# Kernel tuning notes

Measured on AMD Instinct MI355X. Metric: run time of the kernel, lower is better.

Reference implementation:

```python
import jax, jax.numpy as jnp
import numpy as np

DIM = 1024
HEADS = 16
HEAD_DIM = DIM // HEADS


def setup_inputs() -> dict:
    key = jax.random.key(0)
    ks = jax.random.split(key, 5)
    s = 1.0 / np.sqrt(DIM)
    x = jax.random.normal(ks[0], (2, 2048, DIM), dtype=jnp.float32)
    # torch nn.Linear weights are [out_features, in_features]
    W_qkv = jax.random.uniform(ks[1], (3 * DIM, DIM), dtype=jnp.float32, minval=-s, maxval=s)
    b_qkv = jax.random.uniform(ks[2], (3 * DIM,), dtype=jnp.float32, minval=-s, maxval=s)
    W_out = jax.random.uniform(ks[3], (DIM, DIM), dtype=jnp.float32, minval=-s, maxval=s)
    b_out = jax.random.uniform(ks[4], (DIM,), dtype=jnp.float32, minval=-s, maxval=s)
    return {"x": x, "W_qkv": W_qkv, "b_qkv": b_qkv, "W_out": W_out, "b_out": b_out}


def reference(x, W_qkv, b_qkv, W_out, b_out):
    B, N, D = x.shape
    qkv = jnp.einsum('bnd,ed->bne', x, W_qkv) + b_qkv            # [B,N,3D]
    qkv = qkv.reshape(B, N, 3, HEADS, HEAD_DIM)
    qkv = jnp.transpose(qkv, (2, 0, 3, 1, 4))                    # [3,B,H,N,hd]
    q, k, v = qkv[0], qkv[1], qkv[2]
    scale = 1.0 / np.sqrt(HEAD_DIM).astype(np.float32)
    attn = jnp.einsum('bhnd,bhmd->bhnm', q, k) * scale           # [B,H,N,N]
    attn = jax.nn.softmax(attn, axis=-1)
    out = jnp.einsum('bhnm,bhmd->bhnd', attn, v)                 # [B,H,N,hd]
    out = jnp.transpose(out, (0, 2, 1, 3)).reshape(B, N, D)
    out = jnp.einsum('bnd,ed->bne', out, W_out) + b_out
    return out
```

## Files before the change

kernel.cpp:

```cpp
#include <hip/hip_runtime.h>
#include <stdint.h>
#include <stddef.h>

typedef __attribute__((ext_vector_type(4))) float  f32x4;
typedef __attribute__((ext_vector_type(8))) short  s16x8;
typedef __attribute__((ext_vector_type(4))) float  float4v;
typedef __attribute__((ext_vector_type(4))) unsigned short u16x4;
typedef __attribute__((ext_vector_type(2))) unsigned int   u32x2;

#define DIM    1024
#define HEADS  16
#define HD     64
#define SEQ    2048
#define BATCH  2
#define TOKENS (BATCH * SEQ)

#define QSCALE 0.18033688011112042f

__device__ __forceinline__ unsigned short f2bf(float f) {
  union { float f; uint32_t u; } x; x.f = f;
  uint32_t r = x.u + 0x7fffu + ((x.u >> 16) & 1u);
  return (unsigned short)(r >> 16);
}

__device__ __forceinline__ float fast_exp2(float x) {
#if __has_builtin(__builtin_amdgcn_exp2f)
  return __builtin_amdgcn_exp2f(x);
#else
  return exp2f(x);
#endif
}

__device__ __forceinline__ uint32_t pack_bf16_trunc(uint32_t lo, uint32_t hi) {
#if __has_builtin(__builtin_amdgcn_perm)
  return __builtin_amdgcn_perm(hi, lo, 0x07060302u);
#else
  return (hi & 0xffff0000u) | (lo >> 16);
#endif
}

__device__ __forceinline__ void stage16(const unsigned short* gp, unsigned short* lp) {
#if __has_builtin(__builtin_amdgcn_global_load_lds)
  __builtin_amdgcn_global_load_lds((const __attribute__((address_space(1))) void*)gp,
                                   (__attribute__((address_space(3))) void*)lp, 16, 0, 0);
#else
  *(s16x8*)(lp + (threadIdx.x & 63) * 8) = *(const s16x8*)gp;
#endif
}

#define N4_X  (TOKENS * DIM / 4)
#define N4_WQ (3 * DIM * DIM / 4)
#define N4_WO (DIM * DIM / 4)
__global__ __launch_bounds__(256) void mhsa_cast_all(const float* __restrict__ x,
    const float* __restrict__ wq, const float* __restrict__ wo,
    unsigned short* __restrict__ xb, unsigned short* __restrict__ wqb,
    unsigned short* __restrict__ wob) {
  int i = blockIdx.x * 256 + threadIdx.x;
  const float* src; unsigned short* dst; int off;
  if (i < N4_X)              { src = x;  dst = xb;  off = i; }
  else if (i < N4_X + N4_WQ) { src = wq; dst = wqb; off = i - N4_X; }
  else                       { src = wo; dst = wob; off = i - (N4_X + N4_WQ); }
  float4v f = ((const float4v*)src)[off];
  u16x4 o;
  o.x = f2bf(f.x); o.y = f2bf(f.y); o.z = f2bf(f.z); o.w = f2bf(f.w);
  ((u16x4*)dst)[off] = o;
}


__global__ __launch_bounds__(256, 3) void mhsa_gemm_qkv(const unsigned short* __restrict__ A,
    const unsigned short* __restrict__ Bw, const float* __restrict__ bias,
    unsigned short* __restrict__ qws, unsigned short* __restrict__ kws,
    unsigned short* __restrict__ vws) {
  __shared__ unsigned short As[2][128 * 32];
  __shared__ unsigned short Bs[2][128 * 32];
  const int t = threadIdx.x;
  const int w = t >> 6, l = t & 63;
  const int wm = w >> 1, wn = w & 1;
  const int rowBase = blockIdx.y * 128;
  const int colBase = blockIdx.x * 128;
  const int fr = l & 15, q4 = l >> 4, ln = l & 15;
  const int srow = l >> 2;
  const int scol = ((l & 3) ^ (srow & 3)) * 8;

  f32x4 zero = {0.f, 0.f, 0.f, 0.f};
  f32x4 acc[4][4];
  #pragma unroll
  for (int a = 0; a < 4; ++a)
    #pragma unroll
    for (int b = 0; b < 4; ++b) acc[a][b] = zero;

  #pragma unroll
  for (int it = 0; it < 2; ++it) {
    const int c = w * 2 + it;
    stage16(A  + (size_t)(rowBase + c * 16 + srow) * DIM + scol, &As[0][c * 512]);
    stage16(Bw + (size_t)(colBase + c * 16 + srow) * DIM + scol, &Bs[0][c * 512]);
  }
  __syncthreads();

  for (int kt = 0; kt < DIM / 32; ++kt) {
    const int cur = kt & 1, nxt = cur ^ 1;
    if (kt + 1 < DIM / 32) {
      const int k1 = (kt + 1) * 32;
      #pragma unroll
      for (int it = 0; it < 2; ++it) {
        const int c = w * 2 + it;
        stage16(A  + (size_t)(rowBase + c * 16 + srow) * DIM + k1 + scol, &As[nxt][c * 512]);
        stage16(Bw + (size_t)(colBase + c * 16 + srow) * DIM + k1 + scol, &Bs[nxt][c * 512]);
      }
    }
    s16x8 xf[4], wf[4];
    #pragma unroll
    for (int b = 0; b < 4; ++b)
      xf[b] = *(const s16x8*)&As[cur][(wm * 64 + b * 16 + fr) * 32 + ((q4 ^ (fr & 3)) * 8)];
    #pragma unroll
    for (int a = 0; a < 4; ++a)
      wf[a] = *(const s16x8*)&Bs[cur][(wn * 64 + a * 16 + fr) * 32 + ((q4 ^ (fr & 3)) * 8)];
    #pragma unroll
    for (int a = 0; a < 4; ++a)
      #pragma unroll
      for (int b = 0; b < 4; ++b)
        acc[a][b] = __builtin_amdgcn_mfma_f32_16x16x32_bf16(wf[a], xf[b], acc[a][b], 0, 0, 0);
    __syncthreads();
  }

  const int which = colBase >> 10;
  const float sc = (which == 0) ? QSCALE : 1.0f;
  unsigned short* dst = (which == 0) ? qws : ((which == 1) ? kws : vws);

  #pragma unroll
  for (int a = 0; a < 4; ++a) {
    const int e0 = colBase + wn * 64 + a * 16 + q4 * 4;
    const float4v bs4 = *(const float4v*)&bias[e0];
    const int rr0 = e0 & 1023;
    const int h = rr0 >> 6, d0 = rr0 & 63;
    #pragma unroll
    for (int b = 0; b < 4; ++b) {
      const int tok = rowBase + wm * 64 + b * 16 + ln;
      const int bb = tok >> 11, n = tok & 2047;
      if (which != 2) {
        u16x4 pk;
        #pragma unroll
        for (int r = 0; r < 4; ++r) pk[r] = f2bf((acc[a][b][r] + bs4[r]) * sc);
        *(u16x4*)&dst[(((size_t)(bb * HEADS + h)) * SEQ + n) * HD + d0] = pk;
      } else {
        #pragma unroll
        for (int r = 0; r < 4; ++r)
          dst[(((size_t)(bb * HEADS + h)) * HD + d0 + r) * SEQ + n] =
              f2bf(acc[a][b][r] + bs4[r]);
      }
    }
  }
}

__global__ __launch_bounds__(256, 3) void mhsa_gemm_out(const unsigned short* __restrict__ A,
    const unsigned short* __restrict__ Bw, const float* __restrict__ bias,
    float* __restrict__ out) {
  __shared__ unsigned short As[2][64 * 32];
  __shared__ unsigned short Bs[2][128 * 32];
  const int t = threadIdx.x;
  const int w = t >> 6, l = t & 63;
  const int wm = w >> 1, wn = w & 1;
  const int rowBase = blockIdx.y * 64;
  const int colBase = blockIdx.x * 128;
  const int fr = l & 15, q4 = l >> 4, ln = l & 15;
  const int srow = l >> 2;
  const int scol = ((l & 3) ^ (srow & 3)) * 8;

  f32x4 zero = {0.f, 0.f, 0.f, 0.f};
  f32x4 acc[4][2];
  #pragma unroll
  for (int a = 0; a < 4; ++a)
    #pragma unroll
    for (int b = 0; b < 2; ++b) acc[a][b] = zero;

  #pragma unroll
  for (int it = 0; it < 3; ++it) {
    const int s = w * 3 + it;
    if (s < 4) stage16(A  + (size_t)(rowBase + s * 16 + srow) * DIM + scol, &As[0][s * 512]);
    else       stage16(Bw + (size_t)(colBase + (s - 4) * 16 + srow) * DIM + scol, &Bs[0][(s - 4) * 512]);
  }
  __syncthreads();

  for (int kt = 0; kt < DIM / 32; ++kt) {
    const int cur = kt & 1, nxt = cur ^ 1;
    if (kt + 1 < DIM / 32) {
      const int k1 = (kt + 1) * 32;
      #pragma unroll
      for (int it = 0; it < 3; ++it) {
        const int s = w * 3 + it;
        if (s < 4) stage16(A  + (size_t)(rowBase + s * 16 + srow) * DIM + k1 + scol, &As[nxt][s * 512]);
        else       stage16(Bw + (size_t)(colBase + (s - 4) * 16 + srow) * DIM + k1 + scol, &Bs[nxt][(s - 4) * 512]);
      }
    }
    s16x8 xf[2], wf[4];
    #pragma unroll
    for (int b = 0; b < 2; ++b)
      xf[b] = *(const s16x8*)&As[cur][(wm * 32 + b * 16 + fr) * 32 + ((q4 ^ (fr & 3)) * 8)];
    #pragma unroll
    for (int a = 0; a < 4; ++a)
      wf[a] = *(const s16x8*)&Bs[cur][(wn * 64 + a * 16 + fr) * 32 + ((q4 ^ (fr & 3)) * 8)];
    #pragma unroll
    for (int a = 0; a < 4; ++a)
      #pragma unroll
      for (int b = 0; b < 2; ++b)
        acc[a][b] = __builtin_amdgcn_mfma_f32_16x16x32_bf16(wf[a], xf[b], acc[a][b], 0, 0, 0);
    __syncthreads();
  }

  #pragma unroll
  for (int a = 0; a < 4; ++a) {
    const int e0 = colBase + wn * 64 + a * 16 + q4 * 4;
    const float4v bs4 = *(const float4v*)&bias[e0];
    #pragma unroll
    for (int b = 0; b < 2; ++b) {
      const int tok = rowBase + wm * 32 + b * 16 + ln;
      float4v v;
      #pragma unroll
      for (int r = 0; r < 4; ++r) v[r] = acc[a][b][r] + bs4[r];
      *(float4v*)&out[(size_t)tok * DIM + e0] = v;
    }
  }
}

__global__ __launch_bounds__(256, 2) void mhsa_attn(const unsigned short* __restrict__ q,
    const unsigned short* __restrict__ k, const unsigned short* __restrict__ vt,
    unsigned short* __restrict__ o) {
  __shared__ unsigned short QPs[4 * 32 * 72];
  __shared__ unsigned short Ks[2][64 * 64];
  __shared__ unsigned short Vs[2][64 * 64];
  const int t = threadIdx.x, w = t >> 6, l = t & 63;
  const int q4 = l >> 4, ln = l & 15;
  const int bh = blockIdx.y, q0 = blockIdx.x * 128;
  const unsigned short* qb  = q  + (size_t)bh * SEQ * HD;
  const unsigned short* kb  = k  + (size_t)bh * SEQ * HD;
  const unsigned short* vtb = vt + (size_t)bh * HD * SEQ;

  const int srow = l >> 3;
  const int scol = ((l & 7) ^ srow) * 8;

  unsigned short* Pw = &QPs[w * (32 * 72)];

  #pragma unroll
  for (int it = 0; it < 4; ++it)
    stage16(qb + (size_t)(q0 + w * 32 + it * 8 + srow) * HD + scol, &Pw[it * 512]);
  #pragma unroll
  for (int it = 0; it < 2; ++it) {
    const int c = w + it * 4;
    stage16(kb  + (size_t)(c * 8 + srow) * HD + scol, &Ks[0][c * 512]);
    stage16(vtb + (size_t)(c * 8 + srow) * SEQ + scol, &Vs[0][c * 512]);
  }
  __syncthreads();

  s16x8 aq[2][2];
  #pragma unroll
  for (int i = 0; i < 2; ++i)
    #pragma unroll
    for (int kk = 0; kk < 2; ++kk)
      aq[i][kk] = *(const s16x8*)&Pw[(i * 16 + ln) * 64 + (((kk * 4 + q4) ^ (ln & 7)) * 8)];

  f32x4 zero = {0.f, 0.f, 0.f, 0.f};
  f32x4 accO[2][4];
  float lsum[2] = {0.f, 0.f};
  #pragma unroll
  for (int i = 0; i < 2; ++i)
    #pragma unroll
    for (int jd = 0; jd < 4; ++jd) accO[i][jd] = zero;

  for (int jt = 0; jt < SEQ / 64; ++jt) {
    const int cur = jt & 1, nxt = cur ^ 1;
    if (jt + 1 < SEQ / 64) {
      const int j1 = (jt + 1) * 64;
      #pragma unroll
      for (int it = 0; it < 2; ++it) {
        const int c = w + it * 4;
        stage16(kb  + (size_t)(j1 + c * 8 + srow) * HD + scol, &Ks[nxt][c * 512]);
        stage16(vtb + (size_t)(c * 8 + srow) * SEQ + j1 + scol, &Vs[nxt][c * 512]);
      }
    }

    f32x4 St[4][2];
    #pragma unroll
    for (int jb = 0; jb < 4; ++jb)
      #pragma unroll
      for (int i = 0; i < 2; ++i) St[jb][i] = zero;
    #pragma unroll
    for (int jb = 0; jb < 4; ++jb) {
      s16x8 ak0 = *(const s16x8*)&Ks[cur][(jb * 16 + ln) * 64 + ((q4 ^ (ln & 7)) * 8)];
      s16x8 ak1 = *(const s16x8*)&Ks[cur][(jb * 16 + ln) * 64 + (((4 + q4) ^ (ln & 7)) * 8)];
      #pragma unroll
      for (int i = 0; i < 2; ++i) {
        St[jb][i] = __builtin_amdgcn_mfma_f32_16x16x32_bf16(ak0, aq[i][0], St[jb][i], 0, 0, 0);
        St[jb][i] = __builtin_amdgcn_mfma_f32_16x16x32_bf16(ak1, aq[i][1], St[jb][i], 0, 0, 0);
      }
    }

    #pragma unroll
    for (int i = 0; i < 2; ++i)
      #pragma unroll
      for (int jb = 0; jb < 4; ++jb) {
        uint32_t u0 = __float_as_uint(fast_exp2(St[jb][i][0]));
        uint32_t u1 = __float_as_uint(fast_exp2(St[jb][i][1]));
        uint32_t u2 = __float_as_uint(fast_exp2(St[jb][i][2]));
        uint32_t u3 = __float_as_uint(fast_exp2(St[jb][i][3]));
        lsum[i] += __uint_as_float(u0 & 0xffff0000u) + __uint_as_float(u1 & 0xffff0000u)
                 + __uint_as_float(u2 & 0xffff0000u) + __uint_as_float(u3 & 0xffff0000u);
        u32x2 pk;
        pk.x = pack_bf16_trunc(u0, u1);
        pk.y = pack_bf16_trunc(u2, u3);
        *(u32x2*)&Pw[(i * 16 + ln) * 72 + jb * 16 + q4 * 4] = pk;
      }

    s16x8 ap[2][2];
    #pragma unroll
    for (int i = 0; i < 2; ++i)
      #pragma unroll
      for (int kk = 0; kk < 2; ++kk)
        ap[i][kk] = *(const s16x8*)&Pw[(i * 16 + ln) * 72 + kk * 32 + q4 * 8];

    #pragma unroll
    for (int jd = 0; jd < 4; ++jd) {
      s16x8 bv0 = *(const s16x8*)&Vs[cur][(jd * 16 + ln) * 64 + ((q4 ^ (ln & 7)) * 8)];
      s16x8 bv1 = *(const s16x8*)&Vs[cur][(jd * 16 + ln) * 64 + (((4 + q4) ^ (ln & 7)) * 8)];
      #pragma unroll
      for (int i = 0; i < 2; ++i) {
        accO[i][jd] = __builtin_amdgcn_mfma_f32_16x16x32_bf16(ap[i][0], bv0, accO[i][jd], 0, 0, 0);
        accO[i][jd] = __builtin_amdgcn_mfma_f32_16x16x32_bf16(ap[i][1], bv1, accO[i][jd], 0, 0, 0);
      }
    }

    __syncthreads();
  }

  const int b = bh >> 4, h = bh & 15;
  #pragma unroll
  for (int i = 0; i < 2; ++i) {
    float s = lsum[i];
    s += __shfl_xor(s, 16);
    s += __shfl_xor(s, 32);
    const float inv = 1.f / s;
    #pragma unroll
    for (int r = 0; r < 4; ++r) {
      const float invr = __shfl(inv, (l & 48) + q4 * 4 + r);
      const int row = q0 + w * 32 + i * 16 + q4 * 4 + r;
      #pragma unroll
      for (int jd = 0; jd < 4; ++jd)
        o[((size_t)(b * SEQ + row)) * DIM + h * HD + jd * 16 + ln] = f2bf(accO[i][jd][r] * invr);
    }
  }
}

extern "C" void kernel_launch(void* const* d_in, const int* in_sizes, int n_in,
                              void* d_out, int out_size, void* d_ws, size_t ws_size,
                              hipStream_t stream) {
  const float* x     = (const float*)d_in[0];
  const float* Wqkv  = (const float*)d_in[1];
  const float* bqkv  = (const float*)d_in[2];
  const float* Wout  = (const float*)d_in[3];
  const float* bout  = (const float*)d_in[4];
  float* out = (float*)d_out;

  unsigned short* ws = (unsigned short*)d_ws;
  unsigned short* x_bf    = ws;
  unsigned short* wqkv_bf = x_bf    + (size_t)TOKENS * DIM;
  unsigned short* wout_bf = wqkv_bf + (size_t)3 * DIM * DIM;
  unsigned short* q_ws    = wout_bf + (size_t)DIM * DIM;
  unsigned short* k_ws    = q_ws    + (size_t)TOKENS * DIM;
  unsigned short* v_ws    = k_ws    + (size_t)TOKENS * DIM;
  unsigned short* ao_ws   = v_ws    + (size_t)TOKENS * DIM;

  {
    const int n4 = N4_X + N4_WQ + N4_WO;
    mhsa_cast_all<<<n4 / 256, 256, 0, stream>>>(x, Wqkv, Wout, x_bf, wqkv_bf, wout_bf);
  }

  {
    dim3 grid(3 * DIM / 128, TOKENS / 128);
    mhsa_gemm_qkv<<<grid, 256, 0, stream>>>(x_bf, wqkv_bf, bqkv, q_ws, k_ws, v_ws);
  }

  {
    dim3 grid(SEQ / 128, BATCH * HEADS);
    mhsa_attn<<<grid, 256, 0, stream>>>(q_ws, k_ws, v_ws, ao_ws);
  }

  {
    dim3 grid(DIM / 128, TOKENS / 64);
    mhsa_gemm_out<<<grid, 256, 0, stream>>>(ao_ws, wout_bf, bout, out);
  }
}
```

Baseline: 200.6 us.

## Software-pipeline attention loop: compute next QK^T while doing current PV

```diff
diff --git a/kernel.cpp b/kernel.cpp
--- a/kernel.cpp
+++ b/kernel.cpp
@@ -246,8 +246,9 @@
   #pragma unroll
   for (int it = 0; it < 2; ++it) {
     const int c = w + it * 4;
-    stage16(kb  + (size_t)(c * 8 + srow) * HD + scol, &Ks[0][c * 512]);
-    stage16(vtb + (size_t)(c * 8 + srow) * SEQ + scol, &Vs[0][c * 512]);
+    stage16(kb  + (size_t)(c * 8 + srow) * HD + scol,        &Ks[0][c * 512]);
+    stage16(vtb + (size_t)(c * 8 + srow) * SEQ + scol,       &Vs[0][c * 512]);
+    stage16(kb  + (size_t)(64 + c * 8 + srow) * HD + scol,   &Ks[1][c * 512]);
   }
   __syncthreads();
 
@@ -266,18 +267,7 @@
     #pragma unroll
     for (int jd = 0; jd < 4; ++jd) accO[i][jd] = zero;
 
-  for (int jt = 0; jt < SEQ / 64; ++jt) {
-    const int cur = jt & 1, nxt = cur ^ 1;
-    if (jt + 1 < SEQ / 64) {
-      const int j1 = (jt + 1) * 64;
-      #pragma unroll
-      for (int it = 0; it < 2; ++it) {
-        const int c = w + it * 4;
-        stage16(kb  + (size_t)(j1 + c * 8 + srow) * HD + scol, &Ks[nxt][c * 512]);
-        stage16(vtb + (size_t)(c * 8 + srow) * SEQ + j1 + scol, &Vs[nxt][c * 512]);
-      }
-    }
-
+  {
     f32x4 St[4][2];
     #pragma unroll
     for (int jb = 0; jb < 4; ++jb)
@@ -285,15 +275,14 @@
       for (int i = 0; i < 2; ++i) St[jb][i] = zero;
     #pragma unroll
     for (int jb = 0; jb < 4; ++jb) {
-      s16x8 ak0 = *(const s16x8*)&Ks[cur][(jb * 16 + ln) * 64 + ((q4 ^ (ln & 7)) * 8)];
-      s16x8 ak1 = *(const s16x8*)&Ks[cur][(jb * 16 + ln) * 64 + (((4 + q4) ^ (ln & 7)) * 8)];
+      s16x8 ak0 = *(const s16x8*)&Ks[0][(jb * 16 + ln) * 64 + ((q4 ^ (ln & 7)) * 8)];
+      s16x8 ak1 = *(const s16x8*)&Ks[0][(jb * 16 + ln) * 64 + (((4 + q4) ^ (ln & 7)) * 8)];
       #pragma unroll
       for (int i = 0; i < 2; ++i) {
         St[jb][i] = __builtin_amdgcn_mfma_f32_16x16x32_bf16(ak0, aq[i][0], St[jb][i], 0, 0, 0);
         St[jb][i] = __builtin_amdgcn_mfma_f32_16x16x32_bf16(ak1, aq[i][1], St[jb][i], 0, 0, 0);
       }
     }
-
     #pragma unroll
     for (int i = 0; i < 2; ++i)
       #pragma unroll
@@ -309,6 +298,28 @@
         pk.y = pack_bf16_trunc(u2, u3);
         *(u32x2*)&Pw[(i * 16 + ln) * 72 + jb * 16 + q4 * 4] = pk;
       }
+  }
+  __syncthreads();
+
+  const int NT = SEQ / 64;
+  for (int jt = 0; jt < NT; ++jt) {
+    const int cur = jt & 1, nxt = cur ^ 1;
+    if (jt + 2 < NT) {
+      const int j2 = (jt + 2) * 64;
+      #pragma unroll
+      for (int it = 0; it < 2; ++it) {
+        const int c = w + it * 4;
+        stage16(kb + (size_t)(j2 + c * 8 + srow) * HD + scol, &Ks[cur][c * 512]);
+      }
+    }
+    if (jt + 1 < NT) {
+      const int j1 = (jt + 1) * 64;
+      #pragma unroll
+      for (int it = 0; it < 2; ++it) {
+        const int c = w + it * 4;
+        stage16(vtb + (size_t)(c * 8 + srow) * SEQ + j1 + scol, &Vs[nxt][c * 512]);
+      }
+    }
 
     s16x8 ap[2][2];
     #pragma unroll
@@ -317,14 +328,59 @@
       for (int kk = 0; kk < 2; ++kk)
         ap[i][kk] = *(const s16x8*)&Pw[(i * 16 + ln) * 72 + kk * 32 + q4 * 8];
 
-    #pragma unroll
-    for (int jd = 0; jd < 4; ++jd) {
-      s16x8 bv0 = *(const s16x8*)&Vs[cur][(jd * 16 + ln) * 64 + ((q4 ^ (ln & 7)) * 8)];
-      s16x8 bv1 = *(const s16x8*)&Vs[cur][(jd * 16 + ln) * 64 + (((4 + q4) ^ (ln & 7)) * 8)];
-      #pragma unroll
-      for (int i = 0; i < 2; ++i) {
-        accO[i][jd] = __builtin_amdgcn_mfma_f32_16x16x32_bf16(ap[i][0], bv0, accO[i][jd], 0, 0, 0);
-        accO[i][jd] = __builtin_amdgcn_mfma_f32_16x16x32_bf16(ap[i][1], bv1, accO[i][jd], 0, 0, 0);
+    if (jt + 1 < NT) {
+      f32x4 St[4][2];
+      #pragma unroll
+      for (int jb = 0; jb < 4; ++jb)
+        #pragma unroll
+        for (int i = 0; i < 2; ++i) St[jb][i] = zero;
+      #pragma unroll
+      for (int jb = 0; jb < 4; ++jb) {
+        s16x8 ak0 = *(const s16x8*)&Ks[nxt][(jb * 16 + ln) * 64 + ((q4 ^ (ln & 7)) * 8)];
+        s16x8 ak1 = *(const s16x8*)&Ks[nxt][(jb * 16 + ln) * 64 + (((4 + q4) ^ (ln & 7)) * 8)];
+        #pragma unroll
+        for (int i = 0; i < 2; ++i) {
+          St[jb][i] = __builtin_amdgcn_mfma_f32_16x16x32_bf16(ak0, aq[i][0], St[jb][i], 0, 0, 0);
+          St[jb][i] = __builtin_amdgcn_mfma_f32_16x16x32_bf16(ak1, aq[i][1], St[jb][i], 0, 0, 0);
+        }
+      }
+
+      #pragma unroll
+      for (int jd = 0; jd < 4; ++jd) {
+        s16x8 bv0 = *(const s16x8*)&Vs[cur][(jd * 16 + ln) * 64 + ((q4 ^ (ln & 7)) * 8)];
+        s16x8 bv1 = *(const s16x8*)&Vs[cur][(jd * 16 + ln) * 64 + (((4 + q4) ^ (ln & 7)) * 8)];
+        #pragma unroll
+        for (int i = 0; i < 2; ++i) {
+          accO[i][jd] = __builtin_amdgcn_mfma_f32_16x16x32_bf16(ap[i][0], bv0, accO[i][jd], 0, 0, 0);
+          accO[i][jd] = __builtin_amdgcn_mfma_f32_16x16x32_bf16(ap[i][1], bv1, accO[i][jd], 0, 0, 0);
+        }
+      }
+
+      #pragma unroll
+      for (int i = 0; i < 2; ++i)
+        #pragma unroll
+        for (int jb = 0; jb < 4; ++jb) {
+          uint32_t u0 = __float_as_uint(fast_exp2(St[jb][i][0]));
+          uint32_t u1 = __float_as_uint(fast_exp2(St[jb][i][1]));
+          uint32_t u2 = __float_as_uint(fast_exp2(St[jb][i][2]));
+          uint32_t u3 = __float_as_uint(fast_exp2(St[jb][i][3]));
+          lsum[i] += __uint_as_float(u0 & 0xffff0000u) + __uint_as_float(u1 & 0xffff0000u)
+                   + __uint_as_float(u2 & 0xffff0000u) + __uint_as_float(u3 & 0xffff0000u);
+          u32x2 pk;
+          pk.x = pack_bf16_trunc(u0, u1);
+          pk.y = pack_bf16_trunc(u2, u3);
+          *(u32x2*)&Pw[(i * 16 + ln) * 72 + jb * 16 + q4 * 4] = pk;
+        }
+    } else {
+      #pragma unroll
+      for (int jd = 0; jd < 4; ++jd) {
+        s16x8 bv0 = *(const s16x8*)&Vs[cur][(jd * 16 + ln) * 64 + ((q4 ^ (ln & 7)) * 8)];
+        s16x8 bv1 = *(const s16x8*)&Vs[cur][(jd * 16 + ln) * 64 + (((4 + q4) ^ (ln & 7)) * 8)];
+        #pragma unroll
+        for (int i = 0; i < 2; ++i) {
+          accO[i][jd] = __builtin_amdgcn_mfma_f32_16x16x32_bf16(ap[i][0], bv0, accO[i][jd], 0, 0, 0);
+          accO[i][jd] = __builtin_amdgcn_mfma_f32_16x16x32_bf16(ap[i][1], bv1, accO[i][jd], 0, 0, 0);
+        }
       }
     }
 
```

New measurement: 193.1 us. -3.7%, faster.
